# Kernel tuning notes

Hardware: AMD Instinct MI355X
Metric: run time of the kernel (lower is better)

Reference implementation:

```python
import jax, jax.numpy as jnp
import numpy as np
import math

EMB_DIM = 2048
HEAD_NUMS = 16
HEAD_DIM = EMB_DIM // HEAD_NUMS


def setup_inputs() -> dict:
    key = jax.random.key(0)
    k1, k2, k3, k4, k5 = jax.random.split(key, 5)
    B, S = 2, 2048
    X = jax.random.normal(k1, (B, S, EMB_DIM), dtype=jnp.float32)
    mask = jnp.ones((B, S), dtype=jnp.int32)
    # torch nn.Linear weights: [out_features, in_features]
    W_qkv = jax.random.normal(k2, (3 * EMB_DIM, EMB_DIM), dtype=jnp.float32) / math.sqrt(EMB_DIM)
    b_qkv = jax.random.normal(k3, (3 * EMB_DIM,), dtype=jnp.float32) * 0.01
    W_o = jax.random.normal(k4, (EMB_DIM, EMB_DIM), dtype=jnp.float32) / math.sqrt(EMB_DIM)
    b_o = jax.random.normal(k5, (EMB_DIM,), dtype=jnp.float32) * 0.01
    return {"X": X, "mask": mask, "W_qkv": W_qkv, "b_qkv": b_qkv, "W_o": W_o, "b_o": b_o}


def _rope_tables(seq_len):
    # Bug-faithful to source: exponent divides by full emb_dim, not head_dim.
    angle = 1.0 / jnp.power(10000.0, jnp.arange(0, HEAD_DIM, 2, dtype=jnp.float32) / EMB_DIM)
    t = jnp.arange(seq_len, dtype=jnp.float32)
    freqs = t[:, None] * angle[None, :]            # [S, HEAD_DIM//2]
    freqs = jnp.repeat(freqs, 2, axis=-1)          # [S, HEAD_DIM] (repeat_interleave)
    return jnp.cos(freqs), jnp.sin(freqs)


def _trans(x):
    # de-interleave pairs, then concat([-odd, even]) along last dim (as in source)
    B, H, S, D = x.shape
    xr = x.reshape(B, H, S, D // 2, 2)
    x1, x2 = xr[..., 0], xr[..., 1]
    return jnp.concatenate([-x2, x1], axis=-1)


def reference(X, mask, W_qkv, b_qkv, W_o, b_o):
    B, S, E = X.shape
    cos, sin = _rope_tables(S)                      # [S, HEAD_DIM]
    qkv = X @ W_qkv.T + b_qkv                       # [B, S, 3E]
    qkv = qkv.reshape(B, S, 3, HEAD_NUMS, HEAD_DIM).transpose(2, 0, 3, 1, 4)
    Q, K, V = qkv[0], qkv[1], qkv[2]                # [B, H, S, D]
    c = cos[None, None, :, :]
    s = sin[None, None, :, :]
    Q = c * Q + s * _trans(Q)
    K = c * K + s * _trans(K)
    scores = jnp.einsum('bhqd,bhkd->bhqk', Q, K) / math.sqrt(HEAD_DIM)
    pad = mask[:, None, None, :]                    # [B,1,1,S]
    scores = jnp.where(pad == 0, -1e9, scores)
    attn = jax.nn.softmax(scores, axis=-1)          # dropout = identity (eval)
    out = jnp.einsum('bhqk,bhkd->bhqd', attn, V)    # [B,H,S,D]
    out = out.transpose(0, 2, 1, 3).reshape(B, S, E)
    return out @ W_o.T + b_o
```

## Files before the change

kernel.cpp:

```cpp
#include <hip/hip_runtime.h>
#include <hip/hip_bf16.h>
#include <math.h>

typedef __bf16 bf16x8 __attribute__((ext_vector_type(8)));
typedef float  f32x4  __attribute__((ext_vector_type(4)));
typedef float  f32x16 __attribute__((ext_vector_type(16)));
typedef unsigned short ushort_t;
typedef ushort_t us4 __attribute__((ext_vector_type(4)));

#define MFMA16(a, b, c) __builtin_amdgcn_mfma_f32_16x16x32_bf16((a), (b), (c), 0, 0, 0)
#define MFMA32(a, b, c) __builtin_amdgcn_mfma_f32_32x32x16_bf16((a), (b), (c), 0, 0, 0)

__device__ __forceinline__ float bf2f(ushort_t h) {
    union { unsigned u; float f; } v; v.u = ((unsigned)h) << 16; return v.f;
}
__device__ __forceinline__ ushort_t f2bf(float x) {
    union { float f; unsigned u; } v; v.f = x;
    unsigned r = v.u + 0x7FFFu + ((v.u >> 16) & 1u);
    return (ushort_t)(r >> 16);
}
__device__ __forceinline__ void gl2lds16(const void* g, void* l) {
    __builtin_amdgcn_global_load_lds((__attribute__((address_space(1))) void*)(g),
                                     (__attribute__((address_space(3))) void*)(l),
                                     16, 0, 0);
}

__global__ __launch_bounds__(256) void detect_kernel(const ushort_t* __restrict__ w, int* flag)
{
    __shared__ int cnt[256];
    const int t = threadIdx.x;
    int c = 0;
    for (int i = t; i < 65536; i += 256) {
        const unsigned hw = w[i];
        const unsigned e = (hw >> 7) & 0xFFu;
        if (e == 0xFFu || (e == 0u && (hw & 0x7Fu) != 0u)) c++;
    }
    cnt[t] = c;
    __syncthreads();
    for (int s = 128; s > 0; s >>= 1) {
        if (t < s) cnt[t] += cnt[t + s];
        __syncthreads();
    }
    if (t == 0) flag[0] = (cnt[0] >= 8) ? 1 : 0;
}

__global__ __launch_bounds__(256) void convert_all_kernel(
    const void* __restrict__ X,    const void* __restrict__ Wqkv,
    const void* __restrict__ bqkv, const void* __restrict__ Wo,
    const void* __restrict__ bo,
    ushort_t* __restrict__ Xc,    ushort_t* __restrict__ Wqkvc,
    ushort_t* __restrict__ bqkvc, ushort_t* __restrict__ Woc,
    ushort_t* __restrict__ boc,   const int* __restrict__ flag)
{
    int blk = blockIdx.x;
    const void* src; ushort_t* dst; int n;
    if (blk < 4096)          { src = X;    dst = Xc;    n = 8388608; }
    else if (blk < 10240)    { blk -= 4096;  src = Wqkv; dst = Wqkvc; n = 12582912; }
    else if (blk < 10243)    { blk -= 10240; src = bqkv; dst = bqkvc; n = 6144; }
    else if (blk < 12291)    { blk -= 10243; src = Wo;   dst = Woc;   n = 4194304; }
    else                     { blk -= 12291; src = bo;   dst = boc;   n = 2048; }

    const int i0 = (blk * 256 + threadIdx.x) * 8;
    if (i0 + 8 > n) return;
    if (flag[0]) {
        const f32x4 a = *(const f32x4*)((const float*)src + i0);
        const f32x4 b = *(const f32x4*)((const float*)src + i0 + 4);
        ushort_t o[8];
        o[0]=f2bf(a[0]); o[1]=f2bf(a[1]); o[2]=f2bf(a[2]); o[3]=f2bf(a[3]);
        o[4]=f2bf(b[0]); o[5]=f2bf(b[1]); o[6]=f2bf(b[2]); o[7]=f2bf(b[3]);
        *(bf16x8*)(dst + i0) = *(const bf16x8*)o;
    } else {
        *(bf16x8*)(dst + i0) = *(const bf16x8*)((const ushort_t*)src + i0);
    }
}

__global__ __launch_bounds__(512, 2) void gemm256_bt_bias(
    const ushort_t* __restrict__ A, const ushort_t* __restrict__ B,
    const ushort_t* __restrict__ bias, ushort_t* __restrict__ C,
    int M, int N, int K)
{
    __shared__ __align__(16) ushort_t SM[65536];
    const int tid = threadIdx.x;
    const int l = tid & 63, ln = l & 15, q2 = l >> 4;
    const int w = tid >> 6, wm = w >> 2, wn = w & 3;
    const int m0 = blockIdx.y * 256, n0 = blockIdx.x * 256;
    const int NT = K >> 6;

#define STG_A256(slot, kbase, o) do { \
    const int s_ = (o) * 512 + tid; const int r_ = s_ >> 2; \
    const int q_ = (s_ & 3) ^ ((r_ >> 1) & 3); \
    gl2lds16(A + (size_t)(m0 + r_) * K + (kbase) + q_ * 8, \
             SM + (slot) * 16384 + s_ * 8); } while (0)
#define STG_B256(slot, kbase, o) do { \
    const int s_ = (o) * 512 + tid; const int r_ = s_ >> 2; \
    const int q_ = (s_ & 3) ^ ((r_ >> 1) & 3); \
    gl2lds16(B + (size_t)(n0 + r_) * K + (kbase) + q_ * 8, \
             SM + (slot) * 16384 + 8192 + s_ * 8); } while (0)
#define DSA256(slot, row) (*(const bf16x8*)(SM + (slot) * 16384 + (row) * 32 + ((q2 ^ (((row) >> 1) & 3)) << 3)))
#define DSB256(slot, row) (*(const bf16x8*)(SM + (slot) * 16384 + 8192 + (row) * 32 + ((q2 ^ (((row) >> 1) & 3)) << 3)))
#define BAR256() asm volatile("s_barrier" ::: "memory")

    f32x4 acc[8][4];
    const f32x4 z4 = {0.f, 0.f, 0.f, 0.f};
#pragma unroll
    for (int i = 0; i < 8; i++)
#pragma unroll
        for (int j = 0; j < 4; j++) acc[i][j] = z4;

    STG_A256(0, 0, 0);  STG_A256(0, 0, 1);  STG_B256(0, 0, 0);  STG_B256(0, 0, 1);
    STG_A256(1, 32, 0); STG_A256(1, 32, 1); STG_B256(1, 32, 0); STG_B256(1, 32, 1);
    if (NT > 1) STG_A256(2, 64, 0);
    asm volatile("s_waitcnt vmcnt(5)" ::: "memory");
    BAR256();

    for (int t = 0; t < NT; ++t) {
        const int s0 = (2 * t) & 3, s1 = (2 * t + 1) & 3;
        const int sA = (2 * t + 2) & 3, sB = (2 * t + 3) & 3;
        const int kA = (t + 1) << 6, kB = kA + 32, kC = (t + 2) << 6;
        const bool stAB = (t < NT - 1), stC = (t < NT - 2);
        const int rA0 = wm * 128, rA1 = wm * 128 + 64, rB = wn * 64;
        bf16x8 a0[4], a1[4], b00[2], b01[2], b10[2], b11[2];

#pragma unroll
        for (int ii = 0; ii < 4; ii++) a0[ii] = DSA256(s0, rA0 + ii * 16 + ln);
        b00[0] = DSB256(s0, rB + ln);
        b00[1] = DSB256(s0, rB + 16 + ln);
        if (stAB) STG_A256(sA, kA, 1);
        __builtin_amdgcn_s_setprio(1);
#pragma unroll
        for (int ii = 0; ii < 4; ii++) {
            acc[ii][0] = MFMA16(a0[ii], b00[0], acc[ii][0]);
            acc[ii][1] = MFMA16(a0[ii], b00[1], acc[ii][1]);
        }
        __builtin_amdgcn_s_setprio(0);
        if (stAB) { asm volatile("s_waitcnt vmcnt(2)" ::: "memory"); }
        else      { asm volatile("s_waitcnt vmcnt(0)" ::: "memory"); }
        BAR256();

#pragma unroll
        for (int ii = 0; ii < 4; ii++) a1[ii] = DSA256(s1, rA0 + ii * 16 + ln);
        b01[0] = DSB256(s1, rB + ln);
        b01[1] = DSB256(s1, rB + 16 + ln);
        if (stAB) STG_B256(sA, kA, 0);
        __builtin_amdgcn_s_setprio(1);
#pragma unroll
        for (int ii = 0; ii < 4; ii++) {
            acc[ii][0] = MFMA16(a1[ii], b01[0], acc[ii][0]);
            acc[ii][1] = MFMA16(a1[ii], b01[1], acc[ii][1]);
        }
        __builtin_amdgcn_s_setprio(0);
        BAR256();

        b10[0] = DSB256(s0, rB + 32 + ln);
        b10[1] = DSB256(s0, rB + 48 + ln);
        if (stAB) STG_B256(sA, kA, 1);
        __builtin_amdgcn_s_setprio(1);
#pragma unroll
        for (int ii = 0; ii < 4; ii++) {
            acc[ii][2] = MFMA16(a0[ii], b10[0], acc[ii][2]);
            acc[ii][3] = MFMA16(a0[ii], b10[1], acc[ii][3]);
        }
        __builtin_amdgcn_s_setprio(0);
        BAR256();

        b11[0] = DSB256(s1, rB + 32 + ln);
        b11[1] = DSB256(s1, rB + 48 + ln);
        if (stAB) STG_A256(sB, kB, 0);
        __builtin_amdgcn_s_setprio(1);
#pragma unroll
        for (int ii = 0; ii < 4; ii++) {
            acc[ii][2] = MFMA16(a1[ii], b11[0], acc[ii][2]);
            acc[ii][3] = MFMA16(a1[ii], b11[1], acc[ii][3]);
        }
        __builtin_amdgcn_s_setprio(0);
        BAR256();

#pragma unroll
        for (int ii = 0; ii < 4; ii++) a0[ii] = DSA256(s0, rA1 + ii * 16 + ln);
        if (stAB) STG_A256(sB, kB, 1);
        __builtin_amdgcn_s_setprio(1);
#pragma unroll
        for (int ii = 0; ii < 4; ii++) {
            acc[4 + ii][2] = MFMA16(a0[ii], b10[0], acc[4 + ii][2]);
            acc[4 + ii][3] = MFMA16(a0[ii], b10[1], acc[4 + ii][3]);
        }
        __builtin_amdgcn_s_setprio(0);
        BAR256();

#pragma unroll
        for (int ii = 0; ii < 4; ii++) a1[ii] = DSA256(s1, rA1 + ii * 16 + ln);
        if (stAB) STG_B256(sB, kB, 0);
        __builtin_amdgcn_s_setprio(1);
#pragma unroll
        for (int ii = 0; ii < 4; ii++) {
            acc[4 + ii][2] = MFMA16(a1[ii], b11[0], acc[4 + ii][2]);
            acc[4 + ii][3] = MFMA16(a1[ii], b11[1], acc[4 + ii][3]);
        }
        __builtin_amdgcn_s_setprio(0);
        BAR256();

        if (stAB) STG_B256(sB, kB, 1);
        __builtin_amdgcn_s_setprio(1);
#pragma unroll
        for (int ii = 0; ii < 4; ii++) {
            acc[4 + ii][0] = MFMA16(a0[ii], b00[0], acc[4 + ii][0]);
            acc[4 + ii][1] = MFMA16(a0[ii], b00[1], acc[4 + ii][1]);
        }
        __builtin_amdgcn_s_setprio(0);
        BAR256();

        if (stC) STG_A256(s0, kC, 0);
        __builtin_amdgcn_s_setprio(1);
#pragma unroll
        for (int ii = 0; ii < 4; ii++) {
            acc[4 + ii][0] = MFMA16(a1[ii], b01[0], acc[4 + ii][0]);
            acc[4 + ii][1] = MFMA16(a1[ii], b01[1], acc[4 + ii][1]);
        }
        __builtin_amdgcn_s_setprio(0);
        if (t < NT - 2)       { asm volatile("s_waitcnt vmcnt(5)" ::: "memory"); }
        else if (t == NT - 2) { asm volatile("s_waitcnt vmcnt(4)" ::: "memory"); }
        BAR256();
    }

    __syncthreads();
#pragma unroll
    for (int j = 0; j < 4; j++) {
        const int nloc = wn * 64 + j * 16 + ln;
        const float bv = bf2f(bias[n0 + nloc]);
#pragma unroll
        for (int i = 0; i < 8; i++) {
            const int rloc = wm * 128 + i * 16 + q2 * 4;
#pragma unroll
            for (int r = 0; r < 4; r++)
                SM[(rloc + r) * 256 + nloc] = f2bf(acc[i][j][r] + bv);
        }
    }
    __syncthreads();
#pragma unroll
    for (int k = 0; k < 16; k++) {
        const int e = k * 512 + tid;
        const int row = e >> 5, unit = e & 31;
        *(bf16x8*)(C + (size_t)(m0 + row) * N + n0 + unit * 8) =
            *(const bf16x8*)(SM + row * 256 + unit * 8);
    }
#undef STG_A256
#undef STG_B256
#undef DSA256
#undef DSB256
#undef BAR256
}

__global__ __launch_bounds__(256) void gemm_bt_bias_out(
    const ushort_t* __restrict__ A, const ushort_t* __restrict__ B,
    const ushort_t* __restrict__ bias, void* __restrict__ C,
    int M, int N, int K, const int* __restrict__ flag)
{
    __shared__ __align__(16) ushort_t As[128 * 32];
    __shared__ __align__(16) ushort_t Bs[128 * 32];
    const int tid = threadIdx.x;
    const int w = tid >> 6, l = tid & 63, q = l >> 4, ln = l & 15;
    const int wm = w >> 1, wn = w & 1;
    const int lin = blockIdx.y * 16 + blockIdx.x;
    const int nlin = (lin & 7) * 64 + (lin >> 3);
    const int m0 = (nlin >> 4) * 128, n0 = (nlin & 15) * 128;
    const int sr = tid >> 2;
    const int sc = (tid & 3) * 8;

    f32x4 acc[4][4];
    const f32x4 z4 = {0.f, 0.f, 0.f, 0.f};
    for (int i = 0; i < 4; i++) for (int j = 0; j < 4; j++) acc[i][j] = z4;

    for (int k0 = 0; k0 < K; k0 += 32) {
        __syncthreads();
        gl2lds16(A + (size_t)(m0 + sr) * K + k0 + sc,       As + sr * 32 + sc);
        gl2lds16(A + (size_t)(m0 + 64 + sr) * K + k0 + sc,  As + (64 + sr) * 32 + sc);
        gl2lds16(B + (size_t)(n0 + sr) * K + k0 + sc,       Bs + sr * 32 + sc);
        gl2lds16(B + (size_t)(n0 + 64 + sr) * K + k0 + sc,  Bs + (64 + sr) * 32 + sc);
        __syncthreads();
        bf16x8 a[4], bb[4];
        for (int i = 0; i < 4; i++)
            a[i]  = *(const bf16x8*)(As + (wm * 64 + i * 16 + ln) * 32 + q * 8);
        for (int j = 0; j < 4; j++)
            bb[j] = *(const bf16x8*)(Bs + (wn * 64 + j * 16 + ln) * 32 + q * 8);
        for (int i = 0; i < 4; i++)
            for (int j = 0; j < 4; j++)
                acc[i][j] = MFMA16(a[i], bb[j], acc[i][j]);
    }
    const int f = flag[0];
    for (int j = 0; j < 4; j++) {
        const int n = n0 + wn * 64 + j * 16 + ln;
        const float bv = bf2f(bias[n]);
        for (int i = 0; i < 4; i++) {
            const int mrow = m0 + wm * 64 + i * 16 + q * 4;
            for (int r = 0; r < 4; r++) {
                const float val = acc[i][j][r] + bv;
                const size_t idx = (size_t)(mrow + r) * N + n;
                if (f) ((float*)C)[idx] = val;
                else   ((ushort_t*)C)[idx] = f2bf(val);
            }
        }
    }
}

__global__ __launch_bounds__(256) void rope_vtrans_kernel(ushort_t* qkv,
                                                          ushort_t* __restrict__ Vt)
{
    __shared__ __align__(16) ushort_t lds[64 * 136];
    const int t = threadIdx.x;

    if (blockIdx.x < 4096) {
        const int bs = blockIdx.x;
        const int s = bs & 2047;
        const int qk = t >> 7;
        const int u = t & 127;
        const int h = u >> 3, i = u & 7;
        ushort_t* row = qkv + (size_t)bs * 6144 + qk * 2048 + h * 128;

        union { bf16x8 v; ushort_t e[8]; } L0, L1, L2, L3;
        L0.v = *(const bf16x8*)(row + 8 * i);
        L1.v = *(const bf16x8*)(row + 64 + 8 * i);
        L2.v = *(const bf16x8*)(row + 16 * i);
        L3.v = *(const bf16x8*)(row + 16 * i + 8);

        float* cs = (float*)lds;
        if (t < 64) {
            const float ang = powf(10000.0f, -(float)(2 * t) / 2048.0f);
            float sv, cv;
            sincosf((float)s * ang, &sv, &cv);
            cs[2 * t]     = cv;
            cs[2 * t + 1] = sv;
        }
        __syncthreads();

        float ca[4], sa_[4], cb[4], sb[4];
#pragma unroll
        for (int e = 0; e < 4; e++) {
            ca[e]  = cs[(4 * i + e) * 2];
            sa_[e] = cs[(4 * i + e) * 2 + 1];
            cb[e]  = cs[(32 + 4 * i + e) * 2];
            sb[e]  = cs[(32 + 4 * i + e) * 2 + 1];
        }
        ushort_t oA[8], oB[8];
#pragma unroll
        for (int d = 0; d < 8; d++) {
            const int e = d >> 1;
            const float pA = (d < 4) ? bf2f(L2.e[2 * d + 1]) : bf2f(L3.e[2 * d - 7]);
            const float pB = (d < 4) ? bf2f(L2.e[2 * d])     : bf2f(L3.e[2 * d - 8]);
            oA[d] = f2bf(ca[e] * bf2f(L0.e[d]) - sa_[e] * pA);
            oB[d] = f2bf(cb[e] * bf2f(L1.e[d]) + sb[e] * pB);
        }
        *(bf16x8*)(row + 8 * i)      = *(const bf16x8*)oA;
        *(bf16x8*)(row + 64 + 8 * i) = *(const bf16x8*)oB;
    } else {
        const int blk = blockIdx.x - 4096;
        const int st = blk & 31, h = (blk >> 5) & 15, b = blk >> 9;
#pragma unroll
        for (int i = 0; i < 4; i++) {
            const int e = i * 256 + t;
            const int r = e >> 4, cb2 = e & 15;
            *(bf16x8*)(lds + r * 136 + cb2 * 8) =
                *(const bf16x8*)(qkv + (size_t)(b * 2048 + st * 64 + r) * 6144 + 4096 + h * 128 + cb2 * 8);
        }
        __syncthreads();
        const int d = t >> 1, s0 = (t & 1) * 32;
        const size_t obase = ((size_t)(b * 16 + h) * 128 + d) * 2048 + st * 64 + s0;
#pragma unroll
        for (int q4 = 0; q4 < 4; q4++) {
            ushort_t tmp[8];
#pragma unroll
            for (int j = 0; j < 8; j++) tmp[j] = lds[(s0 + q4 * 8 + j) * 136 + d];
            *(bf16x8*)(Vt + obase + q4 * 8) = *(const bf16x8*)tmp;
        }
    }
}

__global__ __launch_bounds__(256, 2) void flash_kernel(
    const ushort_t* __restrict__ qkv, const ushort_t* __restrict__ Vt,
    const int* __restrict__ mask, ushort_t* __restrict__ AO)
{
    __shared__ __align__(16) ushort_t SM[16384];
    ushort_t* Ks = SM;
    ushort_t* Vs = SM + 8192;
    const int t = threadIdx.x;
    const int w = t >> 6, l = t & 63, lq = l & 31, q2 = l >> 5;
    const int bid = blockIdx.x;
    const int xcd = bid & 7, ii = bid >> 3;
    const int p = xcd * 4 + (ii >> 4);
    const int qb = (ii & 15) * 128;
    const int h = p & 15, b = p >> 4;
    const size_t brow = (size_t)b * 2048;
    const float scale = 0.08838834764831845f;
    const int qrow = qb + w * 32 + lq;
    const size_t vbase = (size_t)(b * 16 + h) * 128;

    bf16x8 qf[8];
#pragma unroll
    for (int kb = 0; kb < 8; kb++)
        qf[kb] = *(const bf16x8*)(qkv + (brow + qrow) * 6144 + h * 128 + kb * 16 + q2 * 8);

    float m_old = -1e30f, lsum = 0.f;
    f32x16 acc_o[4];
#pragma unroll
    for (int dt = 0; dt < 4; dt++)
#pragma unroll
        for (int r = 0; r < 16; r++) acc_o[dt][r] = 0.f;

    bf16x8 kst[4], vst[4];
#pragma unroll
    for (int i = 0; i < 4; i++) {
        const int s_ = i * 256 + t; const int row = s_ >> 4; const int u = s_ & 15;
        kst[i] = *(const bf16x8*)(qkv + (brow + row) * 6144 + 2048 + h * 128 + u * 8);
    }
#pragma unroll
    for (int i = 0; i < 4; i++) {
        const int s_ = i * 256 + t; const int row = s_ >> 3; const int u = s_ & 7;
        vst[i] = *(const bf16x8*)(Vt + (vbase + row) * 2048 + u * 8);
    }

    for (int s0 = 0; s0 < 2048; s0 += 64) {
        const int mk = mask[brow + s0 + l];
        const unsigned long long bm = __ballot(mk != 0);
        asm volatile("s_waitcnt lgkmcnt(0)" ::: "memory");
        asm volatile("s_barrier" ::: "memory");
#pragma unroll
        for (int i = 0; i < 4; i++) {
            const int s_ = i * 256 + t; const int row = s_ >> 4; const int u = s_ & 15;
            *(bf16x8*)(Ks + row * 128 + ((u ^ (row & 15)) << 3)) = kst[i];
        }
#pragma unroll
        for (int i = 0; i < 4; i++) {
            const int s_ = i * 256 + t; const int row = s_ >> 3; const int u = s_ & 7;
            *(bf16x8*)(Vs + row * 64 + ((u ^ (row & 7)) << 3)) = vst[i];
        }
        if (s0 + 64 < 2048) {
#pragma unroll
            for (int i = 0; i < 4; i++) {
                const int s_ = i * 256 + t; const int row = s_ >> 4; const int u = s_ & 15;
                kst[i] = *(const bf16x8*)(qkv + (brow + s0 + 64 + row) * 6144 + 2048 + h * 128 + u * 8);
            }
#pragma unroll
            for (int i = 0; i < 4; i++) {
                const int s_ = i * 256 + t; const int row = s_ >> 3; const int u = s_ & 7;
                vst[i] = *(const bf16x8*)(Vt + (vbase + row) * 2048 + s0 + 64 + u * 8);
            }
        }
        asm volatile("s_waitcnt lgkmcnt(0)" ::: "memory");
        asm volatile("s_barrier" ::: "memory");

        f32x16 sa[2];
#pragma unroll
        for (int mt = 0; mt < 2; mt++) {
#pragma unroll
            for (int r = 0; r < 16; r++) sa[mt][r] = 0.f;
            const int row = mt * 32 + lq;
            __builtin_amdgcn_s_setprio(1);
#pragma unroll
            for (int kb = 0; kb < 8; kb++) {
                bf16x8 a = *(const bf16x8*)(Ks + row * 128 + (((kb * 2 + q2) ^ (row & 15)) << 3));
                sa[mt] = MFMA32(a, qf[kb], sa[mt]);
            }
            __builtin_amdgcn_s_setprio(0);
        }
        float p_[32];
        float mr = -1e30f;
        if (bm == ~0ull) {
#pragma unroll
            for (int mt = 0; mt < 2; mt++)
#pragma unroll
                for (int r = 0; r < 16; r++) {
                    const float v = sa[mt][r] * scale;
                    p_[mt * 16 + r] = v;
                    mr = fmaxf(mr, v);
                }
        } else {
#pragma unroll
            for (int mt = 0; mt < 2; mt++)
#pragma unroll
                for (int r = 0; r < 16; r++) {
                    const int srow = mt * 32 + (r & 3) + 8 * (r >> 2) + 4 * q2;
                    const float bias = ((bm >> srow) & 1ull) ? 0.f : -1e9f;
                    const float v = sa[mt][r] * scale + bias;
                    p_[mt * 16 + r] = v;
                    mr = fmaxf(mr, v);
                }
        }
        mr = fmaxf(mr, __shfl_xor(mr, 32, 64));
        if (!__all(mr <= m_old + 8.0f)) {
            const float mnew = fmaxf(m_old, mr);
            const float alpha = __expf(m_old - mnew);
            lsum *= alpha;
#pragma unroll
            for (int dt = 0; dt < 4; dt++)
#pragma unroll
                for (int r = 0; r < 16; r++) acc_o[dt][r] *= alpha;
            m_old = mnew;
        }
        float rs = 0.f;
#pragma unroll
        for (int i = 0; i < 32; i++) { p_[i] = __expf(p_[i] - m_old); rs += p_[i]; }
        rs += __shfl_xor(rs, 32, 64);
        lsum += rs;

#pragma unroll
        for (int kb = 0; kb < 4; kb++) {
            const int bb = (kb >> 1) * 16 + (kb & 1) * 8;
            unsigned w01, w23, w45, w67;
            asm("v_cvt_pk_bf16_f32 %0, %1, %2" : "=v"(w01) : "v"(p_[bb + 0]), "v"(p_[bb + 1]));
            asm("v_cvt_pk_bf16_f32 %0, %1, %2" : "=v"(w23) : "v"(p_[bb + 2]), "v"(p_[bb + 3]));
            asm("v_cvt_pk_bf16_f32 %0, %1, %2" : "=v"(w45) : "v"(p_[bb + 4]), "v"(p_[bb + 5]));
            asm("v_cvt_pk_bf16_f32 %0, %1, %2" : "=v"(w67) : "v"(p_[bb + 6]), "v"(p_[bb + 7]));
            asm("v_permlane32_swap_b32 %0, %1" : "+v"(w01), "+v"(w45));
            asm("v_permlane32_swap_b32 %0, %1" : "+v"(w23), "+v"(w67));
            union { unsigned u[4]; bf16x8 v8; } pu;
            pu.u[0] = w01; pu.u[1] = w23; pu.u[2] = w45; pu.u[3] = w67;
            __builtin_amdgcn_s_setprio(1);
#pragma unroll
            for (int dt = 0; dt < 4; dt++) {
                const int row = dt * 32 + lq;
                bf16x8 va = *(const bf16x8*)(Vs + row * 64 + (((kb * 2 + q2) ^ (row & 7)) << 3));
                acc_o[dt] = MFMA32(va, pu.v8, acc_o[dt]);
            }
            __builtin_amdgcn_s_setprio(0);
        }
    }
    __syncthreads();
    const float inv = (lsum > 0.f) ? 1.0f / lsum : 0.f;
#pragma unroll
    for (int dt = 0; dt < 4; dt++)
#pragma unroll
        for (int r2 = 0; r2 < 4; r2++) {
            us4 ov;
#pragma unroll
            for (int j = 0; j < 4; j++) ov[j] = f2bf(acc_o[dt][r2 * 4 + j] * inv);
            const int row = w * 32 + lq;
            const int unit = dt * 4 + r2;
            *(us4*)(SM + row * 128 + ((unit ^ (row & 15)) << 3) + q2 * 4) = ov;
        }
    __syncthreads();
#pragma unroll
    for (int i = 0; i < 8; i++) {
        const int rl = i * 4 + (l >> 4), ch = l & 15;
        const int row = w * 32 + rl;
        bf16x8 vv = *(const bf16x8*)(SM + row * 128 + ((ch ^ (row & 15)) << 3));
        *(bf16x8*)(AO + (brow + qb + row) * 2048 + h * 128 + ch * 8) = vv;
    }
}

extern "C" void kernel_launch(void* const* d_in, const int* in_sizes, int n_in,
                              void* d_out, int out_size, void* d_ws, size_t ws_size,
                              hipStream_t stream)
{
    (void)in_sizes; (void)n_in; (void)out_size; (void)ws_size;
    const void* X    = d_in[0];
    const int*  mask = (const int*)d_in[1];
    const void* Wqkv = d_in[2];
    const void* bqkv = d_in[3];
    const void* Wo   = d_in[4];
    const void* bo   = d_in[5];

    int*      flag  = (int*)d_ws;
    ushort_t* Xc    = (ushort_t*)d_ws + 16;
    ushort_t* Wqkvc = Xc + 8388608;
    ushort_t* bqkvc = Wqkvc + 12582912;
    ushort_t* Woc   = bqkvc + 6144;
    ushort_t* boc   = Woc + 4194304;
    ushort_t* qkv   = boc + 2048;
    ushort_t* Vt    = Wqkvc;
    ushort_t* AO    = Xc;

    detect_kernel<<<1, 256, 0, stream>>>((const ushort_t*)Wqkv, flag);
    convert_all_kernel<<<12292, 256, 0, stream>>>(X, Wqkv, bqkv, Wo, bo,
                                                  Xc, Wqkvc, bqkvc, Woc, boc, flag);
    gemm256_bt_bias<<<dim3(6144 / 256, 4096 / 256), 512, 0, stream>>>(Xc, Wqkvc, bqkvc, qkv, 4096, 6144, 2048);
    rope_vtrans_kernel<<<5120, 256, 0, stream>>>(qkv, Vt);
    flash_kernel<<<512, 256, 0, stream>>>(qkv, Vt, mask, AO);
    gemm_bt_bias_out<<<dim3(2048 / 128, 4096 / 128), 256, 0, stream>>>(AO, Woc, boc, d_out, 4096, 2048, 2048, flag);
}
```

Before: 528.2 us.

## Replace output projection GEMM with pipelined 256x256 tile kernel and LDS-staged epilogue

Factors the QKV GEMM's multi-stage pipelined K loop into a macro and reuses it for the output projection, replacing the simple 128x128 single-buffered kernel that synchronised twice per K step. The epilogue stages results through LDS so global stores are coalesced vector writes, in fp32 or bf16 depending on the flag. The larger tiles give only 128 blocks for a 4096x2048 output, which may underfill the GPU's compute units.

```diff
diff --git a/kernel.cpp b/kernel.cpp
--- a/kernel.cpp
+++ b/kernel.cpp
@@ -73,18 +73,6 @@
         *(bf16x8*)(dst + i0) = *(const bf16x8*)((const ushort_t*)src + i0);
     }
 }
-
-__global__ __launch_bounds__(512, 2) void gemm256_bt_bias(
-    const ushort_t* __restrict__ A, const ushort_t* __restrict__ B,
-    const ushort_t* __restrict__ bias, ushort_t* __restrict__ C,
-    int M, int N, int K)
-{
-    __shared__ __align__(16) ushort_t SM[65536];
-    const int tid = threadIdx.x;
-    const int l = tid & 63, ln = l & 15, q2 = l >> 4;
-    const int w = tid >> 6, wm = w >> 2, wn = w & 3;
-    const int m0 = blockIdx.y * 256, n0 = blockIdx.x * 256;
-    const int NT = K >> 6;
 
 #define STG_A256(slot, kbase, o) do { \
     const int s_ = (o) * 512 + tid; const int r_ = s_ >> 2; \
@@ -100,6 +88,125 @@
 #define DSB256(slot, row) (*(const bf16x8*)(SM + (slot) * 16384 + 8192 + (row) * 32 + ((q2 ^ (((row) >> 1) & 3)) << 3)))
 #define BAR256() asm volatile("s_barrier" ::: "memory")
 
+#define GEMM256_KLOOP() \
+    STG_A256(0, 0, 0);  STG_A256(0, 0, 1);  STG_B256(0, 0, 0);  STG_B256(0, 0, 1); \
+    STG_A256(1, 32, 0); STG_A256(1, 32, 1); STG_B256(1, 32, 0); STG_B256(1, 32, 1); \
+    if (NT > 1) STG_A256(2, 64, 0); \
+    asm volatile("s_waitcnt vmcnt(5)" ::: "memory"); \
+    BAR256(); \
+    for (int t = 0; t < NT; ++t) { \
+        const int s0 = (2 * t) & 3, s1 = (2 * t + 1) & 3; \
+        const int sA = (2 * t + 2) & 3, sB = (2 * t + 3) & 3; \
+        const int kA = (t + 1) << 6, kB = kA + 32, kC = (t + 2) << 6; \
+        const bool stAB = (t < NT - 1), stC = (t < NT - 2); \
+        const int rA0 = wm * 128, rA1 = wm * 128 + 64, rB = wn * 64; \
+        bf16x8 a0[4], a1[4], b00[2], b01[2], b10[2], b11[2]; \
+        _Pragma("unroll") \
+        for (int ii = 0; ii < 4; ii++) a0[ii] = DSA256(s0, rA0 + ii * 16 + ln); \
+        b00[0] = DSB256(s0, rB + ln); \
+        b00[1] = DSB256(s0, rB + 16 + ln); \
+        if (stAB) STG_A256(sA, kA, 1); \
+        __builtin_amdgcn_s_setprio(1); \
+        _Pragma("unroll") \
+        for (int ii = 0; ii < 4; ii++) { \
+            acc[ii][0] = MFMA16(a0[ii], b00[0], acc[ii][0]); \
+            acc[ii][1] = MFMA16(a0[ii], b00[1], acc[ii][1]); \
+        } \
+        __builtin_amdgcn_s_setprio(0); \
+        if (stAB) { asm volatile("s_waitcnt vmcnt(2)" ::: "memory"); } \
+        else      { asm volatile("s_waitcnt vmcnt(0)" ::: "memory"); } \
+        BAR256(); \
+        _Pragma("unroll") \
+        for (int ii = 0; ii < 4; ii++) a1[ii] = DSA256(s1, rA0 + ii * 16 + ln); \
+        b01[0] = DSB256(s1, rB + ln); \
+        b01[1] = DSB256(s1, rB + 16 + ln); \
+        if (stAB) STG_B256(sA, kA, 0); \
+        __builtin_amdgcn_s_setprio(1); \
+        _Pragma("unroll") \
+        for (int ii = 0; ii < 4; ii++) { \
+            acc[ii][0] = MFMA16(a1[ii], b01[0], acc[ii][0]); \
+            acc[ii][1] = MFMA16(a1[ii], b01[1], acc[ii][1]); \
+        } \
+        __builtin_amdgcn_s_setprio(0); \
+        BAR256(); \
+        b10[0] = DSB256(s0, rB + 32 + ln); \
+        b10[1] = DSB256(s0, rB + 48 + ln); \
+        if (stAB) STG_B256(sA, kA, 1); \
+        __builtin_amdgcn_s_setprio(1); \
+        _Pragma("unroll") \
+        for (int ii = 0; ii < 4; ii++) { \
+            acc[ii][2] = MFMA16(a0[ii], b10[0], acc[ii][2]); \
+            acc[ii][3] = MFMA16(a0[ii], b10[1], acc[ii][3]); \
+        } \
+        __builtin_amdgcn_s_setprio(0); \
+        BAR256(); \
+        b11[0] = DSB256(s1, rB + 32 + ln); \
+        b11[1] = DSB256(s1, rB + 48 + ln); \
+        if (stAB) STG_A256(sB, kB, 0); \
+        __builtin_amdgcn_s_setprio(1); \
+        _Pragma("unroll") \
+        for (int ii = 0; ii < 4; ii++) { \
+            acc[ii][2] = MFMA16(a1[ii], b11[0], acc[ii][2]); \
+            acc[ii][3] = MFMA16(a1[ii], b11[1], acc[ii][3]); \
+        } \
+        __builtin_amdgcn_s_setprio(0); \
+        BAR256(); \
+        _Pragma("unroll") \
+        for (int ii = 0; ii < 4; ii++) a0[ii] = DSA256(s0, rA1 + ii * 16 + ln); \
+        if (stAB) STG_A256(sB, kB, 1); \
+        __builtin_amdgcn_s_setprio(1); \
+        _Pragma("unroll") \
+        for (int ii = 0; ii < 4; ii++) { \
+            acc[4 + ii][2] = MFMA16(a0[ii], b10[0], acc[4 + ii][2]); \
+            acc[4 + ii][3] = MFMA16(a0[ii], b10[1], acc[4 + ii][3]); \
+        } \
+        __builtin_amdgcn_s_setprio(0); \
+        BAR256(); \
+        _Pragma("unroll") \
+        for (int ii = 0; ii < 4; ii++) a1[ii] = DSA256(s1, rA1 + ii * 16 + ln); \
+        if (stAB) STG_B256(sB, kB, 0); \
+        __builtin_amdgcn_s_setprio(1); \
+        _Pragma("unroll") \
+        for (int ii = 0; ii < 4; ii++) { \
+            acc[4 + ii][2] = MFMA16(a1[ii], b11[0], acc[4 + ii][2]); \
+            acc[4 + ii][3] = MFMA16(a1[ii], b11[1], acc[4 + ii][3]); \
+        } \
+        __builtin_amdgcn_s_setprio(0); \
+        BAR256(); \
+        if (stAB) STG_B256(sB, kB, 1); \
+        __builtin_amdgcn_s_setprio(1); \
+        _Pragma("unroll") \
+        for (int ii = 0; ii < 4; ii++) { \
+            acc[4 + ii][0] = MFMA16(a0[ii], b00[0], acc[4 + ii][0]); \
+            acc[4 + ii][1] = MFMA16(a0[ii], b00[1], acc[4 + ii][1]); \
+        } \
+        __builtin_amdgcn_s_setprio(0); \
+        BAR256(); \
+        if (stC) STG_A256(s0, kC, 0); \
+        __builtin_amdgcn_s_setprio(1); \
+        _Pragma("unroll") \
+        for (int ii = 0; ii < 4; ii++) { \
+            acc[4 + ii][0] = MFMA16(a1[ii], b01[0], acc[4 + ii][0]); \
+            acc[4 + ii][1] = MFMA16(a1[ii], b01[1], acc[4 + ii][1]); \
+        } \
+        __builtin_amdgcn_s_setprio(0); \
+        if (t < NT - 2)       { asm volatile("s_waitcnt vmcnt(5)" ::: "memory"); } \
+        else if (t == NT - 2) { asm volatile("s_waitcnt vmcnt(4)" ::: "memory"); } \
+        BAR256(); \
+    }
+
+__global__ __launch_bounds__(512, 2) void gemm256_bt_bias(
+    const ushort_t* __restrict__ A, const ushort_t* __restrict__ B,
+    const ushort_t* __restrict__ bias, ushort_t* __restrict__ C,
+    int M, int N, int K)
+{
+    __shared__ __align__(16) ushort_t SM[65536];
+    const int tid = threadIdx.x;
+    const int l = tid & 63, ln = l & 15, q2 = l >> 4;
+    const int w = tid >> 6, wm = w >> 2, wn = w & 3;
+    const int m0 = blockIdx.y * 256, n0 = blockIdx.x * 256;
+    const int NT = K >> 6;
+
     f32x4 acc[8][4];
     const f32x4 z4 = {0.f, 0.f, 0.f, 0.f};
 #pragma unroll
@@ -107,120 +214,7 @@
 #pragma unroll
         for (int j = 0; j < 4; j++) acc[i][j] = z4;
 
-    STG_A256(0, 0, 0);  STG_A256(0, 0, 1);  STG_B256(0, 0, 0);  STG_B256(0, 0, 1);
-    STG_A256(1, 32, 0); STG_A256(1, 32, 1); STG_B256(1, 32, 0); STG_B256(1, 32, 1);
-    if (NT > 1) STG_A256(2, 64, 0);
-    asm volatile("s_waitcnt vmcnt(5)" ::: "memory");
-    BAR256();
-
-    for (int t = 0; t < NT; ++t) {
-        const int s0 = (2 * t) & 3, s1 = (2 * t + 1) & 3;
-        const int sA = (2 * t + 2) & 3, sB = (2 * t + 3) & 3;
-        const int kA = (t + 1) << 6, kB = kA + 32, kC = (t + 2) << 6;
-        const bool stAB = (t < NT - 1), stC = (t < NT - 2);
-        const int rA0 = wm * 128, rA1 = wm * 128 + 64, rB = wn * 64;
-        bf16x8 a0[4], a1[4], b00[2], b01[2], b10[2], b11[2];
-
-#pragma unroll
-        for (int ii = 0; ii < 4; ii++) a0[ii] = DSA256(s0, rA0 + ii * 16 + ln);
-        b00[0] = DSB256(s0, rB + ln);
-        b00[1] = DSB256(s0, rB + 16 + ln);
-        if (stAB) STG_A256(sA, kA, 1);
-        __builtin_amdgcn_s_setprio(1);
-#pragma unroll
-        for (int ii = 0; ii < 4; ii++) {
-            acc[ii][0] = MFMA16(a0[ii], b00[0], acc[ii][0]);
-            acc[ii][1] = MFMA16(a0[ii], b00[1], acc[ii][1]);
-        }
-        __builtin_amdgcn_s_setprio(0);
-        if (stAB) { asm volatile("s_waitcnt vmcnt(2)" ::: "memory"); }
-        else      { asm volatile("s_waitcnt vmcnt(0)" ::: "memory"); }
-        BAR256();
-
-#pragma unroll
-        for (int ii = 0; ii < 4; ii++) a1[ii] = DSA256(s1, rA0 + ii * 16 + ln);
-        b01[0] = DSB256(s1, rB + ln);
-        b01[1] = DSB256(s1, rB + 16 + ln);
-        if (stAB) STG_B256(sA, kA, 0);
-        __builtin_amdgcn_s_setprio(1);
-#pragma unroll
-        for (int ii = 0; ii < 4; ii++) {
-            acc[ii][0] = MFMA16(a1[ii], b01[0], acc[ii][0]);
-            acc[ii][1] = MFMA16(a1[ii], b01[1], acc[ii][1]);
-        }
-        __builtin_amdgcn_s_setprio(0);
-        BAR256();
-
-        b10[0] = DSB256(s0, rB + 32 + ln);
-        b10[1] = DSB256(s0, rB + 48 + ln);
-        if (stAB) STG_B256(sA, kA, 1);
-        __builtin_amdgcn_s_setprio(1);
-#pragma unroll
-        for (int ii = 0; ii < 4; ii++) {
-            acc[ii][2] = MFMA16(a0[ii], b10[0], acc[ii][2]);
-            acc[ii][3] = MFMA16(a0[ii], b10[1], acc[ii][3]);
-        }
-        __builtin_amdgcn_s_setprio(0);
-        BAR256();
-
-        b11[0] = DSB256(s1, rB + 32 + ln);
-        b11[1] = DSB256(s1, rB + 48 + ln);
-        if (stAB) STG_A256(sB, kB, 0);
-        __builtin_amdgcn_s_setprio(1);
-#pragma unroll
-        for (int ii = 0; ii < 4; ii++) {
-            acc[ii][2] = MFMA16(a1[ii], b11[0], acc[ii][2]);
-            acc[ii][3] = MFMA16(a1[ii], b11[1], acc[ii][3]);
-        }
-        __builtin_amdgcn_s_setprio(0);
-        BAR256();
-
-#pragma unroll
-        for (int ii = 0; ii < 4; ii++) a0[ii] = DSA256(s0, rA1 + ii * 16 + ln);
-        if (stAB) STG_A256(sB, kB, 1);
-        __builtin_amdgcn_s_setprio(1);
-#pragma unroll
-        for (int ii = 0; ii < 4; ii++) {
-            acc[4 + ii][2] = MFMA16(a0[ii], b10[0], acc[4 + ii][2]);
-            acc[4 + ii][3] = MFMA16(a0[ii], b10[1], acc[4 + ii][3]);
-        }
-        __builtin_amdgcn_s_setprio(0);
-        BAR256();
-
-#pragma unroll
-        for (int ii = 0; ii < 4; ii++) a1[ii] = DSA256(s1, rA1 + ii * 16 + ln);
-        if (stAB) STG_B256(sB, kB, 0);
-        __builtin_amdgcn_s_setprio(1);
-#pragma unroll
-        for (int ii = 0; ii < 4; ii++) {
-            acc[4 + ii][2] = MFMA16(a1[ii], b11[0], acc[4 + ii][2]);
-            acc[4 + ii][3] = MFMA16(a1[ii], b11[1], acc[4 + ii][3]);
-        }
-        __builtin_amdgcn_s_setprio(0);
-        BAR256();
-
-        if (stAB) STG_B256(sB, kB, 1);
-        __builtin_amdgcn_s_setprio(1);
-#pragma unroll
-        for (int ii = 0; ii < 4; ii++) {
-            acc[4 + ii][0] = MFMA16(a0[ii], b00[0], acc[4 + ii][0]);
-            acc[4 + ii][1] = MFMA16(a0[ii], b00[1], acc[4 + ii][1]);
-        }
-        __builtin_amdgcn_s_setprio(0);
-        BAR256();
-
-        if (stC) STG_A256(s0, kC, 0);
-        __builtin_amdgcn_s_setprio(1);
-#pragma unroll
-        for (int ii = 0; ii < 4; ii++) {
-            acc[4 + ii][0] = MFMA16(a1[ii], b01[0], acc[4 + ii][0]);
-            acc[4 + ii][1] = MFMA16(a1[ii], b01[1], acc[4 + ii][1]);
-        }
-        __builtin_amdgcn_s_setprio(0);
-        if (t < NT - 2)       { asm volatile("s_waitcnt vmcnt(5)" ::: "memory"); }
-        else if (t == NT - 2) { asm volatile("s_waitcnt vmcnt(4)" ::: "memory"); }
-        BAR256();
-    }
+    GEMM256_KLOOP();
 
     __syncthreads();
 #pragma unroll
@@ -243,61 +237,79 @@
         *(bf16x8*)(C + (size_t)(m0 + row) * N + n0 + unit * 8) =
             *(const bf16x8*)(SM + row * 256 + unit * 8);
     }
-#undef STG_A256
-#undef STG_B256
-#undef DSA256
-#undef DSB256
-#undef BAR256
-}
-
-__global__ __launch_bounds__(256) void gemm_bt_bias_out(
+}
+
+__global__ __launch_bounds__(512, 2) void gemm256_bt_bias_out(
     const ushort_t* __restrict__ A, const ushort_t* __restrict__ B,
     const ushort_t* __restrict__ bias, void* __restrict__ C,
     int M, int N, int K, const int* __restrict__ flag)
 {
-    __shared__ __align__(16) ushort_t As[128 * 32];
-    __shared__ __align__(16) ushort_t Bs[128 * 32];
+    __shared__ __align__(16) ushort_t SM[65536];
     const int tid = threadIdx.x;
-    const int w = tid >> 6, l = tid & 63, q = l >> 4, ln = l & 15;
-    const int wm = w >> 1, wn = w & 1;
-    const int lin = blockIdx.y * 16 + blockIdx.x;
-    const int nlin = (lin & 7) * 64 + (lin >> 3);
-    const int m0 = (nlin >> 4) * 128, n0 = (nlin & 15) * 128;
-    const int sr = tid >> 2;
-    const int sc = (tid & 3) * 8;
-
-    f32x4 acc[4][4];
+    const int l = tid & 63, ln = l & 15, q2 = l >> 4;
+    const int w = tid >> 6, wm = w >> 2, wn = w & 3;
+    const int m0 = blockIdx.y * 256, n0 = blockIdx.x * 256;
+    const int NT = K >> 6;
+
+    f32x4 acc[8][4];
     const f32x4 z4 = {0.f, 0.f, 0.f, 0.f};
-    for (int i = 0; i < 4; i++) for (int j = 0; j < 4; j++) acc[i][j] = z4;
-
-    for (int k0 = 0; k0 < K; k0 += 32) {
+#pragma unroll
+    for (int i = 0; i < 8; i++)
+#pragma unroll
+        for (int j = 0; j < 4; j++) acc[i][j] = z4;
+
+    GEMM256_KLOOP();
+
+    const int f = flag[0];
+    __syncthreads();
+    if (f) {
+        float* SMf = (float*)SM;
+#pragma unroll
+        for (int p = 0; p < 2; p++) {
+            if (wm == p) {
+#pragma unroll
+                for (int j = 0; j < 4; j++) {
+                    const int nloc = wn * 64 + j * 16 + ln;
+                    const float bv = bf2f(bias[n0 + nloc]);
+#pragma unroll
+                    for (int i = 0; i < 8; i++) {
+                        const int rloc = i * 16 + q2 * 4;
+#pragma unroll
+                        for (int r = 0; r < 4; r++)
+                            SMf[(rloc + r) * 256 + nloc] = acc[i][j][r] + bv;
+                    }
+                }
+            }
+            __syncthreads();
+#pragma unroll
+            for (int k = 0; k < 16; k++) {
+                const int e = k * 512 + tid;
+                const int row = e >> 6, u = e & 63;
+                *(f32x4*)((float*)C + (size_t)(m0 + p * 128 + row) * N + n0 + u * 4) =
+                    *(const f32x4*)(SMf + row * 256 + u * 4);
+            }
+            if (p == 0) __syncthreads();
+        }
+    } else {
+#pragma unroll
+        for (int j = 0; j < 4; j++) {
+            const int nloc = wn * 64 + j * 16 + ln;
+            const float bv = bf2f(bias[n0 + nloc]);
+#pragma unroll
+            for (int i = 0; i < 8; i++) {
+                const int rloc = wm * 128 + i * 16 + q2 * 4;
+#pragma unroll
+                for (int r = 0; r < 4; r++)
+                    SM[(rloc + r) * 256 + nloc] = f2bf(acc[i][j][r] + bv);
+            }
+        }
         __syncthreads();
-        gl2lds16(A + (size_t)(m0 + sr) * K + k0 + sc,       As + sr * 32 + sc);
-        gl2lds16(A + (size_t)(m0 + 64 + sr) * K + k0 + sc,  As + (64 + sr) * 32 + sc);
-        gl2lds16(B + (size_t)(n0 + sr) * K + k0 + sc,       Bs + sr * 32 + sc);
-        gl2lds16(B + (size_t)(n0 + 64 + sr) * K + k0 + sc,  Bs + (64 + sr) * 32 + sc);
-        __syncthreads();
-        bf16x8 a[4], bb[4];
-        for (int i = 0; i < 4; i++)
-            a[i]  = *(const bf16x8*)(As + (wm * 64 + i * 16 + ln) * 32 + q * 8);
-        for (int j = 0; j < 4; j++)
-            bb[j] = *(const bf16x8*)(Bs + (wn * 64 + j * 16 + ln) * 32 + q * 8);
-        for (int i = 0; i < 4; i++)
-            for (int j = 0; j < 4; j++)
-                acc[i][j] = MFMA16(a[i], bb[j], acc[i][j]);
-    }
-    const int f = flag[0];
-    for (int j = 0; j < 4; j++) {
-        const int n = n0 + wn * 64 + j * 16 + ln;
-        const float bv = bf2f(bias[n]);
-        for (int i = 0; i < 4; i++) {
-            const int mrow = m0 + wm * 64 + i * 16 + q * 4;
-            for (int r = 0; r < 4; r++) {
-                const float val = acc[i][j][r] + bv;
-                const size_t idx = (size_t)(mrow + r) * N + n;
-                if (f) ((float*)C)[idx] = val;
-                else   ((ushort_t*)C)[idx] = f2bf(val);
-            }
+#pragma unroll
+        for (int k = 0; k < 16; k++) {
+            const int e = k * 512 + tid;
+            const int row = e >> 5, unit = e & 31;
+            *(bf16x8*)((ushort_t*)C + (size_t)(m0 + row) * N + n0 + unit * 8) =
+                *(const bf16x8*)(SM + row * 256 + unit * 8);
         }
     }
 }
@@ -574,5 +586,5 @@
     gemm256_bt_bias<<<dim3(6144 / 256, 4096 / 256), 512, 0, stream>>>(Xc, Wqkvc, bqkvc, qkv, 4096, 6144, 2048);
     rope_vtrans_kernel<<<5120, 256, 0, stream>>>(qkv, Vt);
     flash_kernel<<<512, 256, 0, stream>>>(qkv, Vt, mask, AO);
-    gemm_bt_bias_out<<<dim3(2048 / 128, 4096 / 128), 256, 0, stream>>>(AO, Woc, boc, d_out, 4096, 2048, 2048, flag);
-}
+    gemm256_bt_bias_out<<<dim3(2048 / 256, 4096 / 256), 512, 0, stream>>>(AO, Woc, boc, d_out, 4096, 2048, 2048, flag);
+}
```

After: 525.5 us. Within noise of the previous version (-0.5%).
